# Kernel optimization log

Measured on AMD Instinct MI355X. Metric: run time of the kernel, lower is better.

## Reference

```python
import jax, jax.numpy as jnp
from jax import lax
import numpy as np

B, C_IN, C_OUT, H, W = 16, 64, 64, 160, 160
K, STRIDE, PAD, DIL, SHIFT = 3, 1, 1, 1, 1


def setup_inputs() -> dict:
    key = jax.random.key(0)
    kx, kw = jax.random.split(key)
    x = jax.random.normal(kx, (B, C_IN, H, W), dtype=jnp.float32)
    weight = jax.random.normal(kw, (C_OUT, C_IN, K, K), dtype=jnp.float32)
    return {"x": x, "weight": weight}


def reference(x, weight):
    Bn, C, Hh, Ww = x.shape
    # zero-pad spatially by shift_distance on all sides (matches F.pad)
    xp = jnp.pad(x, ((0, 0), (0, 0), (SHIFT, SHIFT), (SHIFT, SHIFT)))
    Hp, Wp = Hh + 2 * SHIFT, Ww + 2 * SHIFT
    # shifts list: (dx, dy) for channel groups c % 5
    dxs = jnp.array([0, SHIFT, 0, -SHIFT, 0])
    dys = jnp.array([0, 0, SHIFT, 0, -SHIFT])
    cmod = jnp.arange(C) % 5
    dy = dys[cmod]  # [C] roll along H (dim 2)
    dx = dxs[cmod]  # [C] roll along W (dim 3)
    # torch.roll semantics: out[h, w] = in[(h - dy) % Hp, (w - dx) % Wp]
    row = (jnp.arange(Hp)[None, :] - dy[:, None]) % Hp  # [C, Hp]
    col = (jnp.arange(Wp)[None, :] - dx[:, None]) % Wp  # [C, Wp]
    # single fused gather over channel-dependent row/col indices
    x_shifted = xp[:, jnp.arange(C)[:, None, None], row[:, :, None], col[:, None, :]]
    out = lax.conv_general_dilated(
        x_shifted, weight,
        window_strides=(STRIDE, STRIDE),
        padding=((PAD, PAD), (PAD, PAD)),
        rhs_dilation=(DIL, DIL),
        dimension_numbers=("NCHW", "OIHW", "NCHW"),
    )
    # crop the extra border introduced by the pre-pad
    return out[:, :, 1:-1, 1:-1]
```

## Files before the change

### kernel.cpp

```cpp
#include <hip/hip_runtime.h>
#include <hip/hip_bf16.h>

#define BATCH 16
#define CIN 64
#define COUT 64
#define HH 160
#define WW 160
#define HP 162
#define WP 162

typedef __attribute__((ext_vector_type(8))) __bf16 bf16x8;
typedef __attribute__((ext_vector_type(4))) float f32x4;

__global__ __launch_bounds__(256) void shift_cvt(const float* __restrict__ x,
                                                 unsigned short* __restrict__ xs) {
  __shared__ float lds[64 * 160];
  int y = blockIdx.x % HP;
  int b = blockIdx.x / HP;
  int tid = threadIdx.x;

#pragma unroll
  for (int it = 0; it < 10; ++it) {
    int idx = it * 256 + tid;
    int c = idx / 40;
    int j = idx - c * 40;
    int cm = c % 5;
    int dx = (cm == 1) ? 1 : ((cm == 3) ? -1 : 0);
    int dy = (cm == 2) ? 1 : ((cm == 4) ? -1 : 0);
    int yy = y - dy;
    f32x4 v = {0.f, 0.f, 0.f, 0.f};
    if (yy >= 1 && yy <= HH)
      v = *reinterpret_cast<const f32x4*>(
          x + (((size_t)(b * CIN + c)) * HH + (size_t)(yy - 1)) * WW + j * 4);
    int rot = (c & 31) + dx;
    if (rot < 0) rot += 160;
    int p0 = 4 * j + rot;
#pragma unroll
    for (int e = 0; e < 4; ++e) {
      int p = p0 + e;
      if (p >= 160) p -= 160;
      lds[c * 160 + p] = v[e];
    }
  }
  __syncthreads();

  int c = tid & 63;
  int wv = tid >> 6;
  int cm = c % 5;
  int dx = (cm == 1) ? 1 : ((cm == 3) ? -1 : 0);
  int rot = (c & 31) + dx;
  if (rot < 0) rot += 160;
  size_t obase = ((size_t)(b * HP + y) * WP) * CIN + c;
  const float* lrow = &lds[c * 160];
  for (int xi = wv; xi < WP; xi += 4) {
    int xx = xi - dx - 1;
    float v = 0.f;
    if (xx >= 0 && xx < WW) {
      int p = xx + rot;
      if (p >= 160) p -= 160;
      v = lrow[p];
    }
    __hip_bfloat16 h = __float2bfloat16(v);
    xs[obase + (size_t)xi * CIN] = *reinterpret_cast<unsigned short*>(&h);
  }
}

__global__ __launch_bounds__(256) void wcvt(const float* __restrict__ w,
                                            unsigned short* __restrict__ wb) {
  int e = blockIdx.x * 256 + threadIdx.x;
  if (e >= 9 * 64 * 64) return;
  int tap = e >> 12;
  int o = (e >> 6) & 63;
  int c = e & 63;
  float v = w[((size_t)(o * 64 + c)) * 9 + tap];
  __hip_bfloat16 h = __float2bfloat16(v);
  wb[e] = *reinterpret_cast<unsigned short*>(&h);
}

__global__ __launch_bounds__(256, 3) void conv_mfma(const unsigned short* __restrict__ xs,
                                                    const unsigned short* __restrict__ wb,
                                                    float* __restrict__ out) {
  __shared__ unsigned short lds_in[340 * 72];

  int tj = blockIdx.x, ti = blockIdx.y, b = blockIdx.z;
  int tid = threadIdx.x;
  int y0 = ti * 8, x0 = tj * 32;

  const size_t xs_b = (size_t)b * HP * WP * CIN;
#pragma unroll
  for (int k = 0; k < 11; ++k) {
    int u = k * 256 + tid;
    if (u < 2720) {
      int p = u >> 3, q8 = u & 7;
      int pr = p / 34, pc = p - pr * 34;
      uint4 v = *reinterpret_cast<const uint4*>(
          xs + xs_b + ((size_t)(y0 + pr) * WP + (size_t)(x0 + pc)) * CIN + q8 * 8);
      *reinterpret_cast<uint4*>(&lds_in[p * 72 + q8 * 8]) = v;
    }
  }
  __syncthreads();

  int wv = tid >> 6;
  int lane = tid & 63;
  int l15 = lane & 15;
  int q = lane >> 4;

  const unsigned short* abase = &lds_in[(2 * wv * 34 + l15) * 72 + q * 8];
  const unsigned short* bbase = wb + l15 * 64 + q * 8;

  f32x4 acc[4][4];
#pragma unroll
  for (int a = 0; a < 4; ++a)
#pragma unroll
    for (int bb = 0; bb < 4; ++bb) acc[a][bb] = (f32x4){0.f, 0.f, 0.f, 0.f};

#pragma unroll
  for (int ch = 0; ch < 2; ++ch) {
#pragma unroll
    for (int ky = 0; ky < 3; ++ky) {
#pragma unroll
      for (int kx = 0; kx < 3; ++kx) {
        int tap = ky * 3 + kx;
        bf16x8 Bf[4];
#pragma unroll
        for (int nt = 0; nt < 4; ++nt)
          Bf[nt] = *reinterpret_cast<const bf16x8*>(bbase + tap * 4096 + nt * 1024 + ch * 32);
        bf16x8 A[4];
#pragma unroll
        for (int mt = 0; mt < 4; ++mt)
          A[mt] = *reinterpret_cast<const bf16x8*>(
              abase + ((((mt >> 1) + ky) * 34 + kx + (mt & 1) * 16) * 72 + ch * 32));
#pragma unroll
        for (int mt = 0; mt < 4; ++mt)
#pragma unroll
          for (int nt = 0; nt < 4; ++nt)
            acc[mt][nt] = __builtin_amdgcn_mfma_f32_16x16x32_bf16(A[mt], Bf[nt], acc[mt][nt], 0, 0, 0);
      }
    }
  }

#pragma unroll
  for (int mt = 0; mt < 4; ++mt) {
    int i = y0 + 2 * wv + (mt >> 1);
    int xo = x0 + (mt & 1) * 16 + q * 4;
#pragma unroll
    for (int nt = 0; nt < 4; ++nt) {
      int o = nt * 16 + l15;
      *reinterpret_cast<f32x4*>(out + ((size_t)(b * COUT + o) * HH + (size_t)i) * WW + xo) =
          acc[mt][nt];
    }
  }
}

extern "C" void kernel_launch(void* const* d_in, const int* in_sizes, int n_in,
                              void* d_out, int out_size, void* d_ws, size_t ws_size,
                              hipStream_t stream) {
  const float* x = (const float*)d_in[0];
  const float* w = (const float*)d_in[1];
  float* out = (float*)d_out;

  unsigned short* xs = (unsigned short*)d_ws;
  unsigned short* wb = (unsigned short*)((char*)d_ws + (size_t)BATCH * HP * WP * CIN * 2);

  hipLaunchKernelGGL(shift_cvt, dim3(BATCH * HP), dim3(256), 0, stream, x, xs);
  hipLaunchKernelGGL(wcvt, dim3(144), dim3(256), 0, stream, w, wb);
  hipLaunchKernelGGL(conv_mfma, dim3(5, 20, BATCH), dim3(256), 0, stream, xs, wb, out);
}
```

Before: 278.3 us.

## Merge prep kernels, vectorize shifted stores, async LDS loads with swizzle, pipeline fragments

Folds the weight conversion into the shift/convert kernel, removing one launch. The shifted-input write now emits 8 channels per 16-byte store instead of scalar 2-byte stores. The conv kernel loads its input tile with global_load_lds into an XOR-swizzled unpadded LDS layout, which avoids bank conflicts and register staging. It also double- and triple-buffers the A and B fragments across the 18 K-steps to overlap loads with MFMA. The cost is more register pressure and correctness that depends on the swizzle and LDS-DMA addressing.

```diff
diff --git a/kernel.cpp b/kernel.cpp
--- a/kernel.cpp
+++ b/kernel.cpp
@@ -11,10 +11,30 @@
 
 typedef __attribute__((ext_vector_type(8))) __bf16 bf16x8;
 typedef __attribute__((ext_vector_type(4))) float f32x4;
-
-__global__ __launch_bounds__(256) void shift_cvt(const float* __restrict__ x,
-                                                 unsigned short* __restrict__ xs) {
+typedef __attribute__((ext_vector_type(8))) unsigned short ushort8;
+
+typedef __attribute__((address_space(1))) const unsigned int gu32;
+typedef __attribute__((address_space(3))) unsigned int lu32;
+
+__global__ __launch_bounds__(256) void prep(const float* __restrict__ x,
+                                            const float* __restrict__ w,
+                                            unsigned short* __restrict__ xs,
+                                            unsigned short* __restrict__ wb) {
   __shared__ float lds[64 * 160];
+
+  if (blockIdx.x >= BATCH * HP) {
+    int e = (blockIdx.x - BATCH * HP) * 256 + threadIdx.x;
+    if (e < 9 * 64 * 64) {
+      int tap = e >> 12;
+      int o = (e >> 6) & 63;
+      int c = e & 63;
+      float v = w[((size_t)(o * 64 + c)) * 9 + tap];
+      __hip_bfloat16 h = __float2bfloat16(v);
+      wb[e] = *reinterpret_cast<unsigned short*>(&h);
+    }
+    return;
+  }
+
   int y = blockIdx.x % HP;
   int b = blockIdx.x / HP;
   int tid = threadIdx.x;
@@ -44,43 +64,47 @@
   }
   __syncthreads();
 
-  int c = tid & 63;
-  int wv = tid >> 6;
-  int cm = c % 5;
-  int dx = (cm == 1) ? 1 : ((cm == 3) ? -1 : 0);
-  int rot = (c & 31) + dx;
-  if (rot < 0) rot += 160;
-  size_t obase = ((size_t)(b * HP + y) * WP) * CIN + c;
-  const float* lrow = &lds[c * 160];
-  for (int xi = wv; xi < WP; xi += 4) {
-    int xx = xi - dx - 1;
-    float v = 0.f;
-    if (xx >= 0 && xx < WW) {
-      int p = xx + rot;
-      if (p >= 160) p -= 160;
-      v = lrow[p];
-    }
-    __hip_bfloat16 h = __float2bfloat16(v);
-    xs[obase + (size_t)xi * CIN] = *reinterpret_cast<unsigned short*>(&h);
-  }
-}
-
-__global__ __launch_bounds__(256) void wcvt(const float* __restrict__ w,
-                                            unsigned short* __restrict__ wb) {
-  int e = blockIdx.x * 256 + threadIdx.x;
-  if (e >= 9 * 64 * 64) return;
-  int tap = e >> 12;
-  int o = (e >> 6) & 63;
-  int c = e & 63;
-  float v = w[((size_t)(o * 64 + c)) * 9 + tap];
-  __hip_bfloat16 h = __float2bfloat16(v);
-  wb[e] = *reinterpret_cast<unsigned short*>(&h);
+  int cg = tid & 7;
+  int xr = tid >> 3;
+  int dxe[8], rote[8], rowb[8];
+#pragma unroll
+  for (int e = 0; e < 8; ++e) {
+    int c = cg * 8 + e;
+    int cm = c % 5;
+    int dx = (cm == 1) ? 1 : ((cm == 3) ? -1 : 0);
+    int rot = (c & 31) + dx;
+    if (rot < 0) rot += 160;
+    dxe[e] = dx;
+    rote[e] = rot;
+    rowb[e] = c * 160;
+  }
+  size_t obase = ((size_t)(b * HP + y) * WP) * CIN + cg * 8;
+#pragma unroll
+  for (int it = 0; it < 6; ++it) {
+    int xi = it * 32 + xr;
+    if (xi < WP) {
+      ushort8 val;
+#pragma unroll
+      for (int e = 0; e < 8; ++e) {
+        int xx = xi - dxe[e] - 1;
+        float v = 0.f;
+        if (xx >= 0 && xx < WW) {
+          int p = rote[e] + xx;
+          if (p >= 160) p -= 160;
+          v = lds[rowb[e] + p];
+        }
+        __hip_bfloat16 h = __float2bfloat16(v);
+        val[e] = *reinterpret_cast<unsigned short*>(&h);
+      }
+      *reinterpret_cast<ushort8*>(xs + obase + (size_t)xi * CIN) = val;
+    }
+  }
 }
 
 __global__ __launch_bounds__(256, 3) void conv_mfma(const unsigned short* __restrict__ xs,
                                                     const unsigned short* __restrict__ wb,
                                                     float* __restrict__ out) {
-  __shared__ unsigned short lds_in[340 * 72];
+  __shared__ __align__(16) unsigned short lds_in[340 * 64];
 
   int tj = blockIdx.x, ti = blockIdx.y, b = blockIdx.z;
   int tid = threadIdx.x;
@@ -91,11 +115,13 @@
   for (int k = 0; k < 11; ++k) {
     int u = k * 256 + tid;
     if (u < 2720) {
-      int p = u >> 3, q8 = u & 7;
+      int p = u >> 3;
+      int j = (u & 7) ^ (p & 7);
       int pr = p / 34, pc = p - pr * 34;
-      uint4 v = *reinterpret_cast<const uint4*>(
-          xs + xs_b + ((size_t)(y0 + pr) * WP + (size_t)(x0 + pc)) * CIN + q8 * 8);
-      *reinterpret_cast<uint4*>(&lds_in[p * 72 + q8 * 8]) = v;
+      const unsigned short* src =
+          xs + xs_b + ((size_t)(y0 + pr) * WP + (size_t)(x0 + pc)) * CIN + j * 8;
+      __builtin_amdgcn_global_load_lds((gu32*)src, (lu32*)&lds_in[(u & ~63) * 8],
+                                       16, 0, 0);
     }
   }
   __syncthreads();
@@ -104,40 +130,53 @@
   int lane = tid & 63;
   int l15 = lane & 15;
   int q = lane >> 4;
-
-  const unsigned short* abase = &lds_in[(2 * wv * 34 + l15) * 72 + q * 8];
+  int pb = 2 * wv * 34 + l15;
   const unsigned short* bbase = wb + l15 * 64 + q * 8;
 
   f32x4 acc[4][4];
 #pragma unroll
   for (int a = 0; a < 4; ++a)
 #pragma unroll
-    for (int bb = 0; bb < 4; ++bb) acc[a][bb] = (f32x4){0.f, 0.f, 0.f, 0.f};
-
-#pragma unroll
-  for (int ch = 0; ch < 2; ++ch) {
-#pragma unroll
-    for (int ky = 0; ky < 3; ++ky) {
-#pragma unroll
-      for (int kx = 0; kx < 3; ++kx) {
-        int tap = ky * 3 + kx;
-        bf16x8 Bf[4];
-#pragma unroll
-        for (int nt = 0; nt < 4; ++nt)
-          Bf[nt] = *reinterpret_cast<const bf16x8*>(bbase + tap * 4096 + nt * 1024 + ch * 32);
-        bf16x8 A[4];
-#pragma unroll
-        for (int mt = 0; mt < 4; ++mt)
-          A[mt] = *reinterpret_cast<const bf16x8*>(
-              abase + ((((mt >> 1) + ky) * 34 + kx + (mt & 1) * 16) * 72 + ch * 32));
-#pragma unroll
-        for (int mt = 0; mt < 4; ++mt)
-#pragma unroll
-          for (int nt = 0; nt < 4; ++nt)
-            acc[mt][nt] = __builtin_amdgcn_mfma_f32_16x16x32_bf16(A[mt], Bf[nt], acc[mt][nt], 0, 0, 0);
-      }
-    }
-  }
+    for (int bb2 = 0; bb2 < 4; ++bb2) acc[a][bb2] = (f32x4){0.f, 0.f, 0.f, 0.f};
+
+  bf16x8 Ab[2][4];
+  bf16x8 Bb[3][4];
+
+#define LOAD_B(buf, t)                                                        \
+  {                                                                           \
+    const int ch_ = (t) / 9, tap_ = (t) % 9;                                  \
+    _Pragma("unroll") for (int nt = 0; nt < 4; ++nt)                          \
+        Bb[buf][nt] = *reinterpret_cast<const bf16x8*>(                       \
+            bbase + tap_ * 4096 + nt * 1024 + ch_ * 32);                      \
+  }
+
+#define LOAD_A(buf, t)                                                        \
+  {                                                                           \
+    const int ch_ = (t) / 9, ky_ = ((t) % 9) / 3, kx_ = (t) % 3;              \
+    _Pragma("unroll") for (int mt = 0; mt < 4; ++mt) {                        \
+      int pix = pb + (((mt >> 1) + ky_) * 34 + kx_ + (mt & 1) * 16);          \
+      int chunk = (ch_ * 4 + q) ^ (pix & 7);                                  \
+      Ab[buf][mt] =                                                           \
+          *reinterpret_cast<const bf16x8*>(&lds_in[pix * 64 + chunk * 8]);    \
+    }                                                                         \
+  }
+
+  LOAD_B(0, 0);
+  LOAD_B(1, 1);
+  LOAD_A(0, 0);
+#pragma unroll
+  for (int t = 0; t < 18; ++t) {
+    if (t + 2 < 18) LOAD_B((t + 2) % 3, t + 2);
+    if (t + 1 < 18) LOAD_A((t + 1) & 1, t + 1);
+#pragma unroll
+    for (int mt = 0; mt < 4; ++mt)
+#pragma unroll
+      for (int nt = 0; nt < 4; ++nt)
+        acc[mt][nt] = __builtin_amdgcn_mfma_f32_16x16x32_bf16(
+            Ab[t & 1][mt], Bb[t % 3][nt], acc[mt][nt], 0, 0, 0);
+  }
+#undef LOAD_A
+#undef LOAD_B
 
 #pragma unroll
   for (int mt = 0; mt < 4; ++mt) {
@@ -162,7 +201,6 @@
   unsigned short* xs = (unsigned short*)d_ws;
   unsigned short* wb = (unsigned short*)((char*)d_ws + (size_t)BATCH * HP * WP * CIN * 2);
 
-  hipLaunchKernelGGL(shift_cvt, dim3(BATCH * HP), dim3(256), 0, stream, x, xs);
-  hipLaunchKernelGGL(wcvt, dim3(144), dim3(256), 0, stream, w, wb);
+  hipLaunchKernelGGL(prep, dim3(BATCH * HP + 144), dim3(256), 0, stream, x, w, xs, wb);
   hipLaunchKernelGGL(conv_mfma, dim3(5, 20, BATCH), dim3(256), 0, stream, xs, wb, out);
 }
```

Measured after the change: 276.5 us. No clear change (-0.7%).
